# Kernel tuning notes

Measured on AMD Instinct MI355X. Metric: run time of the kernel, lower is better.

Reference implementation:

```python
import jax, jax.numpy as jnp
import numpy as np

N = 8192   # nodes
F = 128    # feature dim (in_feats == out_feats)
D = 4      # polynomial order / number of theta coefficients


def setup_inputs() -> dict:
    key = jax.random.key(0)
    k_adj, k_feat, k_lapl = jax.random.split(key, 3)
    # normalized adjacency stand-in (dense, values in [0, 1/N) to keep propagation stable)
    adj = jax.random.uniform(k_adj, (N, N), dtype=jnp.float32) / N
    in_feat = jax.random.normal(k_feat, (N, F), dtype=jnp.float32)
    lapl = jax.random.uniform(k_lapl, (N, N), dtype=jnp.float32)  # unused by forward
    theta = jnp.asarray([0.6, 0.3, 0.08, 0.02], dtype=jnp.float32)  # [D]
    return {"adj": adj, "in_feat": in_feat, "lapl": lapl, "theta": theta}


def reference(adj, in_feat, lapl, theta):
    # h = theta[0] * (adj @ feat); then d-1 hops: feat = adj @ feat; h += theta_k * feat
    feat = adj @ in_feat                 # [N, F]
    h = theta[0] * feat
    for k in range(1, D):                # small fixed polynomial order
        feat = adj @ feat
        h = h + theta[k] * feat
    return h
```

## Files before the change

kernel.cpp:

```cpp
#include <hip/hip_runtime.h>
#include <stdint.h>

#define NN 8192
#define FF 128
#define DD 4
#define BM 128
#define BN 128
#define BK 64
#define KSPLIT 16
#define KCHUNK (NN / KSPLIT)

typedef __attribute__((ext_vector_type(8))) short bf16x8;
typedef __attribute__((ext_vector_type(4))) float f32x4;

__device__ __forceinline__ unsigned short f2bf(float f) {
  uint32_t u = __float_as_uint(f);
  u += 0x7fffu + ((u >> 16) & 1u);
  return (unsigned short)(u >> 16);
}

__device__ __forceinline__ void gld_lds16(const void* g, void* l) {
  auto gp = reinterpret_cast<const uint32_t __attribute__((address_space(1)))*>(
      reinterpret_cast<uintptr_t>(g));
  auto lp = reinterpret_cast<uint32_t __attribute__((address_space(3)))*>(
      reinterpret_cast<uintptr_t>(l));
  __builtin_amdgcn_global_load_lds(gp, lp, 16, 0, 0);
}

__global__ void cvt_adj(const float* __restrict__ a, unsigned short* __restrict__ o) {
  size_t i = ((size_t)blockIdx.x * 256 + threadIdx.x) * 8;
  float4 v0 = *(const float4*)(a + i);
  float4 v1 = *(const float4*)(a + i + 4);
  union { unsigned short us[8]; uint4 v; } p;
  p.us[0] = f2bf(v0.x); p.us[1] = f2bf(v0.y); p.us[2] = f2bf(v0.z); p.us[3] = f2bf(v0.w);
  p.us[4] = f2bf(v1.x); p.us[5] = f2bf(v1.y); p.us[6] = f2bf(v1.z); p.us[7] = f2bf(v1.w);
  *(uint4*)(o + i) = p.v;
}

__global__ void cvt_feat(const float* __restrict__ x, unsigned short* __restrict__ xT) {
  __shared__ float tile[32][33];
  int m0 = blockIdx.x * 32;
  int n0 = blockIdx.y * 32;
  int tx = threadIdx.x & 31, ty = threadIdx.x >> 5;
#pragma unroll
  for (int r = 0; r < 4; ++r) {
    int mm = ty + r * 8;
    tile[mm][tx] = x[(size_t)(m0 + mm) * FF + n0 + tx];
  }
  __syncthreads();
#pragma unroll
  for (int r = 0; r < 4; ++r) {
    int nn = ty + r * 8;
    xT[(size_t)(n0 + nn) * NN + m0 + tx] = f2bf(tile[tx][nn]);
  }
}

__global__ __launch_bounds__(256, 4) void gemm_hop(
    const unsigned short* __restrict__ adjb,
    const unsigned short* __restrict__ featT,
    float* __restrict__ parts) {
  __shared__ unsigned short sA[BM * BK];
  __shared__ unsigned short sB[BN * BK];

  const int bx = blockIdx.x;
  const int mt = bx & 63;
  const int ks = bx >> 6;
  const int m0 = mt * BM;
  const int k0 = ks * KCHUNK;

  const int t = threadIdx.x;
  const int w = t >> 6;
  const int l = t & 63;

  uint32_t offA[4], offB[4];
  unsigned short* ldsA[4];
  unsigned short* ldsB[4];
#pragma unroll
  for (int j = 0; j < 4; ++j) {
    uint32_t obase = (uint32_t)w * 4096u + (uint32_t)j * 1024u;
    uint32_t o = obase + (uint32_t)l * 16u;
    uint32_t r = o >> 7;
    uint32_t c = (o >> 4) & 7u;
    uint32_t gc = c ^ (r & 7u);
    ldsA[j] = sA + (obase >> 1);
    ldsB[j] = sB + (obase >> 1);
    offA[j] = (uint32_t)(m0 + r) * (uint32_t)NN + (uint32_t)k0 + gc * 8u;
    offB[j] = r * (uint32_t)NN + (uint32_t)k0 + gc * 8u;
  }

  f32x4 acc[4][4];
#pragma unroll
  for (int i = 0; i < 4; ++i)
#pragma unroll
    for (int j = 0; j < 4; ++j) acc[i][j] = (f32x4){0.f, 0.f, 0.f, 0.f};

  const int wm = w >> 1;
  const int wn = w & 1;
  const int lr = l & 15;
  const int lq = l >> 4;

  for (int kt = 0; kt < KCHUNK; kt += BK) {
#pragma unroll
    for (int j = 0; j < 4; ++j) gld_lds16(adjb + offA[j], ldsA[j]);
#pragma unroll
    for (int j = 0; j < 4; ++j) gld_lds16(featT + offB[j], ldsB[j]);
#pragma unroll
    for (int j = 0; j < 4; ++j) { offA[j] += BK; offB[j] += BK; }
    __syncthreads();
#pragma unroll
    for (int kk = 0; kk < 2; ++kk) {
      bf16x8 af[4], bfr[4];
#pragma unroll
      for (int tm = 0; tm < 4; ++tm) {
        int row = wm * 64 + tm * 16 + lr;
        int ch = (kk * 4 + lq) ^ (row & 7);
        af[tm] = *(const bf16x8*)(sA + row * BK + ch * 8);
      }
#pragma unroll
      for (int tn = 0; tn < 4; ++tn) {
        int row = wn * 64 + tn * 16 + lr;
        int ch = (kk * 4 + lq) ^ (row & 7);
        bfr[tn] = *(const bf16x8*)(sB + row * BK + ch * 8);
      }
#pragma unroll
      for (int tm = 0; tm < 4; ++tm)
#pragma unroll
        for (int tn = 0; tn < 4; ++tn)
          acc[tm][tn] = __builtin_amdgcn_mfma_f32_16x16x32_bf16(
              af[tm], bfr[tn], acc[tm][tn], 0, 0, 0);
    }
    __syncthreads();
  }

  float* pout = parts + (size_t)ks * NN * FF;
#pragma unroll
  for (int tm = 0; tm < 4; ++tm) {
#pragma unroll
    for (int tn = 0; tn < 4; ++tn) {
      int m = m0 + wm * 64 + tm * 16 + lq * 4;
      int n = wn * 64 + tn * 16 + lr;
#pragma unroll
      for (int r = 0; r < 4; ++r)
        pout[(size_t)(m + r) * FF + n] = acc[tm][tn][r];
    }
  }
}

__global__ void finalize_hop(const float* __restrict__ parts, float* __restrict__ h,
                             unsigned short* __restrict__ featT,
                             const float* __restrict__ theta, int hop) {
  __shared__ float tile[32][33];
  int m0 = blockIdx.x * 32;
  int n0 = blockIdx.y * 32;
  int tx = threadIdx.x & 31, ty = threadIdx.x >> 5;
  float th = theta[hop];
#pragma unroll
  for (int r = 0; r < 4; ++r) {
    int mm = ty + r * 8;
    size_t idx = (size_t)(m0 + mm) * FF + n0 + tx;
    float acc = 0.0f;
#pragma unroll
    for (int s = 0; s < KSPLIT; ++s) acc += parts[(size_t)s * NN * FF + idx];
    tile[mm][tx] = acc;
    float hv = th * acc;
    if (hop > 0) hv += h[idx];
    h[idx] = hv;
  }
  if (hop < DD - 1) {
    __syncthreads();
#pragma unroll
    for (int r = 0; r < 4; ++r) {
      int nn = ty + r * 8;
      featT[(size_t)(n0 + nn) * NN + m0 + tx] = f2bf(tile[tx][nn]);
    }
  }
}

extern "C" void kernel_launch(void* const* d_in, const int* in_sizes, int n_in,
                              void* d_out, int out_size, void* d_ws, size_t ws_size,
                              hipStream_t stream) {
  const float* adj = (const float*)d_in[0];
  const float* in_feat = (const float*)d_in[1];
  const float* theta = (const float*)d_in[3];
  float* h = (float*)d_out;

  char* ws = (char*)d_ws;
  unsigned short* adjb = (unsigned short*)ws;
  unsigned short* fTa = (unsigned short*)(ws + (size_t)NN * NN * 2);
  unsigned short* fTb = fTa + (size_t)FF * NN;
  float* parts = (float*)(fTb + (size_t)FF * NN);

  cvt_adj<<<(int)((size_t)NN * NN / (256 * 8)), 256, 0, stream>>>(adj, adjb);
  cvt_feat<<<dim3(NN / 32, FF / 32), 256, 0, stream>>>(in_feat, fTa);

  unsigned short* fin = fTa;
  unsigned short* fout = fTb;
  for (int hop = 0; hop < DD; ++hop) {
    gemm_hop<<<64 * KSPLIT, 256, 0, stream>>>(adjb, fin, parts);
    finalize_hop<<<dim3(NN / 32, FF / 32), 256, 0, stream>>>(parts, h, fout, theta, hop);
    unsigned short* tmp = fin; fin = fout; fout = tmp;
  }
}
```

Measured before the change: 664.1 us.

## Fuse adjacency bf16 conversion into first hop GEMM and split-K reduction into GEMM tail

Drops the standalone adj fp32-to-bf16 pass. The first hop GEMM now reads fp32 adj, converts it in registers, writes the tile to LDS and stores the bf16 copy for later hops. Split-K partials are reduced inside the GEMM by the last-arriving block per row tile, found with an atomic counter. This removes the separate finalize kernels and one full read of adj. Tiles change to BM=64 and KSPLIT=8, and the change adds a counter memset plus threadfence-based cross-block ordering.

New measurement: 1.527 ms. +129.9%, slower.

```diff
diff --git a/kernel.cpp b/kernel.cpp
--- a/kernel.cpp
+++ b/kernel.cpp
@@ -4,11 +4,12 @@
 #define NN 8192
 #define FF 128
 #define DD 4
-#define BM 128
+#define BM 64
 #define BN 128
 #define BK 64
-#define KSPLIT 16
+#define KSPLIT 8
 #define KCHUNK (NN / KSPLIT)
+#define NT (NN / BM)
 
 typedef __attribute__((ext_vector_type(8))) short bf16x8;
 typedef __attribute__((ext_vector_type(4))) float f32x4;
@@ -27,16 +28,6 @@
   __builtin_amdgcn_global_load_lds(gp, lp, 16, 0, 0);
 }
 
-__global__ void cvt_adj(const float* __restrict__ a, unsigned short* __restrict__ o) {
-  size_t i = ((size_t)blockIdx.x * 256 + threadIdx.x) * 8;
-  float4 v0 = *(const float4*)(a + i);
-  float4 v1 = *(const float4*)(a + i + 4);
-  union { unsigned short us[8]; uint4 v; } p;
-  p.us[0] = f2bf(v0.x); p.us[1] = f2bf(v0.y); p.us[2] = f2bf(v0.z); p.us[3] = f2bf(v0.w);
-  p.us[4] = f2bf(v1.x); p.us[5] = f2bf(v1.y); p.us[6] = f2bf(v1.z); p.us[7] = f2bf(v1.w);
-  *(uint4*)(o + i) = p.v;
-}
-
 __global__ void cvt_feat(const float* __restrict__ x, unsigned short* __restrict__ xT) {
   __shared__ float tile[32][33];
   int m0 = blockIdx.x * 32;
@@ -55,16 +46,26 @@
   }
 }
 
-__global__ __launch_bounds__(256, 4) void gemm_hop(
-    const unsigned short* __restrict__ adjb,
+template <bool FIRST>
+__global__ __launch_bounds__(256, 4) void gemm_poly(
+    const float* __restrict__ adjf,
+    const unsigned short* __restrict__ adjb_in,
+    unsigned short* __restrict__ adjb_out,
     const unsigned short* __restrict__ featT,
-    float* __restrict__ parts) {
+    float* __restrict__ parts,
+    float* __restrict__ h,
+    unsigned short* __restrict__ featT_out,
+    const float* __restrict__ theta,
+    unsigned int* __restrict__ cnt,
+    int hop) {
   __shared__ unsigned short sA[BM * BK];
   __shared__ unsigned short sB[BN * BK];
+  __shared__ float ttile[BM][33];
+  __shared__ int sFlag;
 
   const int bx = blockIdx.x;
-  const int mt = bx & 63;
-  const int ks = bx >> 6;
+  const int ks = bx & (KSPLIT - 1);
+  const int mt = bx >> 3;
   const int m0 = mt * BM;
   const int k0 = ks * KCHUNK;
 
@@ -72,8 +73,7 @@
   const int w = t >> 6;
   const int l = t & 63;
 
-  uint32_t offA[4], offB[4];
-  unsigned short* ldsA[4];
+  uint32_t offB[4];
   unsigned short* ldsB[4];
 #pragma unroll
   for (int j = 0; j < 4; ++j) {
@@ -82,15 +82,33 @@
     uint32_t r = o >> 7;
     uint32_t c = (o >> 4) & 7u;
     uint32_t gc = c ^ (r & 7u);
+    ldsB[j] = sB + (obase >> 1);
+    offB[j] = r * (uint32_t)NN + (uint32_t)k0 + gc * 8u;
+  }
+
+  uint32_t offA[2];
+  unsigned short* ldsA[2];
+#pragma unroll
+  for (int j = 0; j < 2; ++j) {
+    uint32_t obase = (uint32_t)w * 2048u + (uint32_t)j * 1024u;
+    uint32_t o = obase + (uint32_t)l * 16u;
+    uint32_t r = o >> 7;
+    uint32_t c = (o >> 4) & 7u;
+    uint32_t gc = c ^ (r & 7u);
     ldsA[j] = sA + (obase >> 1);
-    ldsB[j] = sB + (obase >> 1);
     offA[j] = (uint32_t)(m0 + r) * (uint32_t)NN + (uint32_t)k0 + gc * 8u;
-    offB[j] = r * (uint32_t)NN + (uint32_t)k0 + gc * 8u;
-  }
-
-  f32x4 acc[4][4];
-#pragma unroll
-  for (int i = 0; i < 4; ++i)
+  }
+
+  const int ar = t >> 2;
+  const int ac4 = t & 3;
+  uint32_t aoff = (uint32_t)(m0 + ar) * (uint32_t)NN + (uint32_t)k0 + (uint32_t)ac4 * 16u;
+  const int ch0 = (2 * ac4) ^ (ar & 7);
+  unsigned short* wA0 = sA + ar * BK + ch0 * 8;
+  unsigned short* wA1 = sA + ar * BK + (ch0 ^ 1) * 8;
+
+  f32x4 acc[2][4];
+#pragma unroll
+  for (int i = 0; i < 2; ++i)
 #pragma unroll
     for (int j = 0; j < 4; ++j) acc[i][j] = (f32x4){0.f, 0.f, 0.f, 0.f};
 
@@ -100,19 +118,38 @@
   const int lq = l >> 4;
 
   for (int kt = 0; kt < KCHUNK; kt += BK) {
-#pragma unroll
-    for (int j = 0; j < 4; ++j) gld_lds16(adjb + offA[j], ldsA[j]);
+    if (FIRST) {
+      float4 v0 = *(const float4*)(adjf + aoff);
+      float4 v1 = *(const float4*)(adjf + aoff + 4);
+      float4 v2 = *(const float4*)(adjf + aoff + 8);
+      float4 v3 = *(const float4*)(adjf + aoff + 12);
+      union { unsigned short us[8]; uint4 v; } p0, p1;
+      p0.us[0] = f2bf(v0.x); p0.us[1] = f2bf(v0.y); p0.us[2] = f2bf(v0.z); p0.us[3] = f2bf(v0.w);
+      p0.us[4] = f2bf(v1.x); p0.us[5] = f2bf(v1.y); p0.us[6] = f2bf(v1.z); p0.us[7] = f2bf(v1.w);
+      p1.us[0] = f2bf(v2.x); p1.us[1] = f2bf(v2.y); p1.us[2] = f2bf(v2.z); p1.us[3] = f2bf(v2.w);
+      p1.us[4] = f2bf(v3.x); p1.us[5] = f2bf(v3.y); p1.us[6] = f2bf(v3.z); p1.us[7] = f2bf(v3.w);
+      *(uint4*)wA0 = p0.v;
+      *(uint4*)wA1 = p1.v;
+      *(uint4*)(adjb_out + aoff) = p0.v;
+      *(uint4*)(adjb_out + aoff + 8) = p1.v;
+      aoff += BK;
+    } else {
+#pragma unroll
+      for (int j = 0; j < 2; ++j) gld_lds16(adjb_in + offA[j], ldsA[j]);
+#pragma unroll
+      for (int j = 0; j < 2; ++j) offA[j] += BK;
+    }
 #pragma unroll
     for (int j = 0; j < 4; ++j) gld_lds16(featT + offB[j], ldsB[j]);
 #pragma unroll
-    for (int j = 0; j < 4; ++j) { offA[j] += BK; offB[j] += BK; }
+    for (int j = 0; j < 4; ++j) offB[j] += BK;
     __syncthreads();
 #pragma unroll
     for (int kk = 0; kk < 2; ++kk) {
-      bf16x8 af[4], bfr[4];
-#pragma unroll
-      for (int tm = 0; tm < 4; ++tm) {
-        int row = wm * 64 + tm * 16 + lr;
+      bf16x8 af[2], bfr[4];
+#pragma unroll
+      for (int tm = 0; tm < 2; ++tm) {
+        int row = wm * 32 + tm * 16 + lr;
         int ch = (kk * 4 + lq) ^ (row & 7);
         af[tm] = *(const bf16x8*)(sA + row * BK + ch * 8);
       }
@@ -123,7 +160,7 @@
         bfr[tn] = *(const bf16x8*)(sB + row * BK + ch * 8);
       }
 #pragma unroll
-      for (int tm = 0; tm < 4; ++tm)
+      for (int tm = 0; tm < 2; ++tm)
 #pragma unroll
         for (int tn = 0; tn < 4; ++tn)
           acc[tm][tn] = __builtin_amdgcn_mfma_f32_16x16x32_bf16(
@@ -134,44 +171,56 @@
 
   float* pout = parts + (size_t)ks * NN * FF;
 #pragma unroll
-  for (int tm = 0; tm < 4; ++tm) {
+  for (int tm = 0; tm < 2; ++tm) {
 #pragma unroll
     for (int tn = 0; tn < 4; ++tn) {
-      int m = m0 + wm * 64 + tm * 16 + lq * 4;
+      int m = m0 + wm * 32 + tm * 16 + lq * 4;
       int n = wn * 64 + tn * 16 + lr;
 #pragma unroll
       for (int r = 0; r < 4; ++r)
         pout[(size_t)(m + r) * FF + n] = acc[tm][tn][r];
     }
   }
-}
-
-__global__ void finalize_hop(const float* __restrict__ parts, float* __restrict__ h,
-                             unsigned short* __restrict__ featT,
-                             const float* __restrict__ theta, int hop) {
-  __shared__ float tile[32][33];
-  int m0 = blockIdx.x * 32;
-  int n0 = blockIdx.y * 32;
-  int tx = threadIdx.x & 31, ty = threadIdx.x >> 5;
-  float th = theta[hop];
-#pragma unroll
-  for (int r = 0; r < 4; ++r) {
-    int mm = ty + r * 8;
-    size_t idx = (size_t)(m0 + mm) * FF + n0 + tx;
-    float acc = 0.0f;
-#pragma unroll
-    for (int s = 0; s < KSPLIT; ++s) acc += parts[(size_t)s * NN * FF + idx];
-    tile[mm][tx] = acc;
-    float hv = th * acc;
-    if (hop > 0) hv += h[idx];
-    h[idx] = hv;
-  }
-  if (hop < DD - 1) {
-    __syncthreads();
-#pragma unroll
-    for (int r = 0; r < 4; ++r) {
-      int nn = ty + r * 8;
-      featT[(size_t)(n0 + nn) * NN + m0 + tx] = f2bf(tile[tx][nn]);
+
+  __threadfence();
+  __syncthreads();
+  if (t == 0)
+    sFlag = (atomicAdd(&cnt[hop * NT + mt], 1u) == KSPLIT - 1) ? 1 : 0;
+  __syncthreads();
+  if (!sFlag) return;
+  __threadfence();
+
+  const float th = theta[hop];
+  const bool accum = (hop > 0);
+  const bool writeT = (hop < DD - 1);
+  const int tx = t & 31;
+  const int ty = t >> 5;
+
+#pragma unroll
+  for (int sc = 0; sc < 4; ++sc) {
+    int n = sc * 32 + tx;
+#pragma unroll
+    for (int mp = 0; mp < 8; ++mp) {
+      int m = mp * 8 + ty;
+      size_t idx = (size_t)(m0 + m) * FF + n;
+      float a = 0.f;
+#pragma unroll
+      for (int s = 0; s < KSPLIT; ++s) a += parts[(size_t)s * NN * FF + idx];
+      float hv = th * a;
+      if (accum) hv += h[idx];
+      h[idx] = hv;
+      if (writeT) ttile[m][tx] = a;
+    }
+    if (writeT) {
+      __syncthreads();
+#pragma unroll
+      for (int np = 0; np < 4; ++np) {
+        int j = np * 8 + ty;
+        uint32_t u = (uint32_t)f2bf(ttile[2 * tx][j]) |
+                     ((uint32_t)f2bf(ttile[2 * tx + 1][j]) << 16);
+        *(uint32_t*)(featT_out + (size_t)(sc * 32 + j) * NN + m0 + 2 * tx) = u;
+      }
+      __syncthreads();
     }
   }
 }
@@ -189,15 +238,19 @@
   unsigned short* fTa = (unsigned short*)(ws + (size_t)NN * NN * 2);
   unsigned short* fTb = fTa + (size_t)FF * NN;
   float* parts = (float*)(fTb + (size_t)FF * NN);
-
-  cvt_adj<<<(int)((size_t)NN * NN / (256 * 8)), 256, 0, stream>>>(adj, adjb);
+  unsigned int* cnt = (unsigned int*)(parts + (size_t)KSPLIT * NN * FF);
+
+  hipMemsetAsync(cnt, 0, (size_t)DD * NT * sizeof(unsigned int), stream);
   cvt_feat<<<dim3(NN / 32, FF / 32), 256, 0, stream>>>(in_feat, fTa);
 
-  unsigned short* fin = fTa;
-  unsigned short* fout = fTb;
-  for (int hop = 0; hop < DD; ++hop) {
-    gemm_hop<<<64 * KSPLIT, 256, 0, stream>>>(adjb, fin, parts);
-    finalize_hop<<<dim3(NN / 32, FF / 32), 256, 0, stream>>>(parts, h, fout, theta, hop);
+  gemm_poly<true><<<NT * KSPLIT, 256, 0, stream>>>(
+      adj, nullptr, adjb, fTa, parts, h, fTb, theta, cnt, 0);
+
+  unsigned short* fin = fTb;
+  unsigned short* fout = fTa;
+  for (int hop = 1; hop < DD; ++hop) {
+    gemm_poly<false><<<NT * KSPLIT, 256, 0, stream>>>(
+        nullptr, adjb, nullptr, fin, parts, h, fout, theta, cnt, hop);
     unsigned short* tmp = fin; fin = fout; fout = tmp;
   }
 }
```
